# Kernel optimization log

Measured on AMD Instinct MI355X. Metric: run time of the kernel, lower is better.

## Reference

```python
import jax, jax.numpy as jnp
import numpy as np

N = 100000
E = 3200000
F_IN = 256
HID = 16
N_CLS = 32


def setup_inputs() -> dict:
    key = jax.random.key(0)
    ks = jax.random.split(key, 9)
    x = jax.random.normal(ks[0], (N, F_IN), dtype=jnp.float32)
    edge_index = jax.random.randint(ks[1], (2, E), 0, N, dtype=jnp.int32)
    def glorot(k, fan_in, fan_out):
        s = jnp.sqrt(6.0 / (fan_in + fan_out)).astype(jnp.float32)
        return jax.random.uniform(k, (fan_in, fan_out), jnp.float32, -s, s)
    return {
        "x": x,
        "edge_index": edge_index,
        "W1": glorot(ks[2], F_IN, HID), "b1": jnp.zeros((HID,), jnp.float32),
        "W2": glorot(ks[3], HID, HID), "b2": jnp.zeros((HID,), jnp.float32),
        "W3": glorot(ks[4], HID, N_CLS), "b3": jnp.zeros((N_CLS,), jnp.float32),
    }


def _gcn_conv(h, W, b, src, dst, deg_inv_sqrt):
    # h: [N, d_in] -> [N, d_out]. PyG GCNConv: linear, then D^-1/2 (A+I) D^-1/2 aggregation, then bias.
    h = h @ W                                        # [N, d_out]
    norm = deg_inv_sqrt[src] * deg_inv_sqrt[dst]     # [E]
    msg = h[src] * norm[:, None]                     # [E, d_out]
    agg = jax.ops.segment_sum(msg, dst, num_segments=N)
    # self-loop contribution: norm_ii = deg_inv_sqrt[i]^2
    agg = agg + (deg_inv_sqrt ** 2)[:, None] * h
    return agg + b


def reference(x, edge_index, W1, b1, W2, b2, W3, b3):
    src, dst = edge_index[0], edge_index[1]
    # degree with self-loops (edge weights = 1), computed on dst per PyG gcn_norm
    deg = jax.ops.segment_sum(jnp.ones((E,), jnp.float32), dst, num_segments=N) + 1.0
    deg_inv_sqrt = jax.lax.rsqrt(deg)
    h = jax.nn.elu(_gcn_conv(x, W1, b1, src, dst, deg_inv_sqrt))
    h = jax.nn.elu(_gcn_conv(h, W2, b2, src, dst, deg_inv_sqrt))
    h = jax.nn.elu(_gcn_conv(h, W3, b3, src, dst, deg_inv_sqrt))
    # dropout is identity in eval mode (training=False)
    return jax.nn.log_softmax(h, axis=1)
```

## Files before the change

kernel.cpp:

```cpp
#include <hip/hip_runtime.h>
#include <math.h>

static constexpr int N_NODES = 100000;
static constexpr int N_EDGES = 3200000;
static constexpr int F_INC   = 256;
static constexpr int HIDC    = 16;
static constexpr int NCLS    = 32;

static constexpr int BNODES  = 256;
static constexpr int NBKT    = (N_NODES + BNODES - 1) / BNODES;
static constexpr int CAP     = 9216;
static constexpr int CHUNK   = 4096;
static constexpr int NCHUNK  = (N_EDGES + CHUNK - 1) / CHUNK;
static constexpr int NTILES  = N_NODES / 16;
static constexpr int GLIN1   = (NTILES + 3) / 4;

typedef __attribute__((ext_vector_type(8))) short bf16x8;
typedef __attribute__((ext_vector_type(4))) float f32x4;

__device__ __forceinline__ unsigned pack_bf2(float a, float b) {
    unsigned ua = __float_as_uint(a);
    unsigned ub = __float_as_uint(b);
    ua = (ua + 0x7FFFu + ((ua >> 16) & 1u)) >> 16;
    ub = (ub + 0x7FFFu + ((ub >> 16) & 1u)) & 0xFFFF0000u;
    return ua | ub;
}
__device__ __forceinline__ float bflo(unsigned v) { return __uint_as_float(v << 16); }
__device__ __forceinline__ float bfhi(unsigned v) { return __uint_as_float(v & 0xFFFF0000u); }
__device__ __forceinline__ float elu1(float t) { return t > 0.f ? t : expm1f(t); }

__global__ void k_zero_cur(int* gcur) {
    int i = threadIdx.x;
    if (i < NBKT) gcur[i] = 0;
}

__global__ __launch_bounds__(256) void k_bucklin(const int* __restrict__ src,
                                                 const int* __restrict__ dst,
                                                 int* gcur, unsigned int* __restrict__ slab,
                                                 const float* __restrict__ x,
                                                 const float* __restrict__ W1,
                                                 unsigned* __restrict__ hb) {
    __shared__ int sm[8192];
    int tid = threadIdx.x;
    if (blockIdx.x < NCHUNK) {
        int* hist  = sm;
        int* sc    = sm + 512;
        int* place = sm + 1024;
        int* gbase = sm + 1536;
        unsigned* staging = (unsigned*)(sm + 2048);
        unsigned short* bid = (unsigned short*)(sm + 6144);
        int e0 = blockIdx.x * CHUNK;
        int n = min(CHUNK, N_EDGES - e0);
        hist[tid] = 0; hist[tid + 256] = 0;
        __syncthreads();
        unsigned pay[16];
        int bk[16];
        #pragma unroll
        for (int r = 0; r < 16; ++r) {
            int i = r * 256 + tid;
            bk[r] = -1;
            if (i < n) {
                int e = e0 + i;
                int s = src[e];
                int t = dst[e];
                int b = t >> 8;
                pay[r] = (unsigned)s | ((unsigned)(t & 255) << 24);
                bk[r] = b;
                atomicAdd(&hist[b], 1);
            }
        }
        __syncthreads();
        sc[tid] = hist[tid]; sc[tid + 256] = hist[tid + 256];
        __syncthreads();
        for (int off = 1; off < 512; off <<= 1) {
            int i0 = tid, i1 = tid + 256;
            int v0 = (i0 >= off) ? sc[i0 - off] : 0;
            int v1 = (i1 >= off) ? sc[i1 - off] : 0;
            __syncthreads();
            sc[i0] += v0; sc[i1] += v1;
            __syncthreads();
        }
        {
            int b0 = tid, b1 = tid + 256;
            int o0 = sc[b0] - hist[b0];
            int o1 = sc[b1] - hist[b1];
            place[b0] = o0; place[b1] = o1;
            sc[b0] = o0; sc[b1] = o1;
            if (b0 < NBKT && hist[b0]) gbase[b0] = atomicAdd(&gcur[b0], hist[b0]);
            if (b1 < NBKT && hist[b1]) gbase[b1] = atomicAdd(&gcur[b1], hist[b1]);
        }
        __syncthreads();
        #pragma unroll
        for (int r = 0; r < 16; ++r) {
            if (bk[r] >= 0) {
                int p = atomicAdd(&place[bk[r]], 1);
                staging[p] = pay[r];
                bid[p] = (unsigned short)bk[r];
            }
        }
        __syncthreads();
        for (int i = tid; i < n; i += 256) {
            int b = bid[i];
            int gp = gbase[b] + (i - sc[b]);
            if (gp < CAP) slab[(size_t)b * CAP + gp] = staging[i];
        }
    } else {
        float* dtile = (float*)sm;
        int lane = tid & 63;
        int w = tid >> 6;
        int tile = (blockIdx.x - NCHUNK) * 4 + w;
        if (tile >= NTILES) return;
        int g = lane >> 4;
        int r = lane & 15;
        union { uint4 u; bf16x8 v; } bfr[8];
        #pragma unroll
        for (int m = 0; m < 8; ++m) {
            unsigned uu[4];
            #pragma unroll
            for (int t = 0; t < 4; ++t) {
                int k0 = 32 * m + 8 * g + 2 * t;
                uu[t] = pack_bf2(W1[k0 * HIDC + r], W1[(k0 + 1) * HIDC + r]);
            }
            bfr[m].u = make_uint4(uu[0], uu[1], uu[2], uu[3]);
        }
        const float* xrow = x + (size_t)(tile * 16 + r) * F_INC;
        f32x4 acc = {0.f, 0.f, 0.f, 0.f};
        #pragma unroll
        for (int m = 0; m < 8; ++m) {
            int ks = 32 * m + 8 * g;
            float4 va = *(const float4*)(xrow + ks);
            float4 vb = *(const float4*)(xrow + ks + 4);
            union { uint4 u; bf16x8 v; } af;
            af.u = make_uint4(pack_bf2(va.x, va.y), pack_bf2(va.z, va.w),
                              pack_bf2(vb.x, vb.y), pack_bf2(vb.z, vb.w));
            acc = __builtin_amdgcn_mfma_f32_16x16x32_bf16(af.v, bfr[m].v, acc, 0, 0, 0);
        }
        float* dt = dtile + w * 288;
        #pragma unroll
        for (int t = 0; t < 4; ++t) dt[(4 * g + t) * 18 + r] = acc[t];
        __builtin_amdgcn_s_waitcnt(0);
        int q = lane & 7;
        #pragma unroll
        for (int h = 0; h < 2; ++h) {
            int rr = (lane >> 3) + 8 * h;
            int node = tile * 16 + rr;
            hb[(size_t)node * 8 + q] = pack_bf2(dt[rr * 18 + 2 * q], dt[rr * 18 + 2 * q + 1]);
        }
    }
}

__global__ __launch_bounds__(512) void k_csr(const int* __restrict__ gcur,
                                             unsigned int* __restrict__ slab,
                                             int* __restrict__ rowptr,
                                             int* __restrict__ cnt,
                                             float* __restrict__ dis) {
    __shared__ int hist[BNODES];
    __shared__ int lofs[BNODES];
    __shared__ int place[BNODES];
    __shared__ unsigned int reord[CAP];
    int tid = threadIdx.x, b = blockIdx.x;
    if (tid < BNODES) hist[tid] = 0;
    __syncthreads();
    int count = min(gcur[b], CAP);
    unsigned int* sl = slab + (size_t)b * CAP;
    for (int i = tid; i < count; i += 512) atomicAdd(&hist[sl[i] >> 24], 1);
    __syncthreads();
    if (tid < BNODES) lofs[tid] = hist[tid];
    __syncthreads();
    for (int off = 1; off < BNODES; off <<= 1) {
        int v = 0;
        if (tid < BNODES && tid >= off) v = lofs[tid - off];
        __syncthreads();
        if (tid < BNODES) lofs[tid] += v;
        __syncthreads();
    }
    if (tid < BNODES) {
        int ex = lofs[tid] - hist[tid];
        lofs[tid] = ex;
        place[tid] = ex;
        int node = b * BNODES + tid;
        if (node < N_NODES) {
            rowptr[node] = b * CAP + ex;
            cnt[node] = hist[tid];
            dis[node] = rsqrtf((float)hist[tid] + 1.0f);
        }
    }
    __syncthreads();
    for (int i = tid; i < count; i += 512) {
        unsigned int v = sl[i];
        int dl = v >> 24;
        int p = atomicAdd(&place[dl], 1);
        reord[p] = v & 0xFFFFFFu;
    }
    __syncthreads();
    for (int i = tid; i < count; i += 512) sl[i] = reord[i];
}

__device__ __forceinline__ void gather4(int base, int deg, int q,
                                        const unsigned* __restrict__ csr,
                                        const unsigned* __restrict__ hb,
                                        float& a0, float& a1, float& a2, float& a3) {
    int j = 0;
    for (; j + 3 < deg; j += 4) {
        int s0 = csr[base + j];
        int s1 = csr[base + j + 1];
        int s2 = csr[base + j + 2];
        int s3 = csr[base + j + 3];
        uint2 v0 = *(const uint2*)&hb[(size_t)s0 * 8 + 2 * q];
        uint2 v1 = *(const uint2*)&hb[(size_t)s1 * 8 + 2 * q];
        uint2 v2 = *(const uint2*)&hb[(size_t)s2 * 8 + 2 * q];
        uint2 v3 = *(const uint2*)&hb[(size_t)s3 * 8 + 2 * q];
        a0 += (bflo(v0.x) + bflo(v1.x)) + (bflo(v2.x) + bflo(v3.x));
        a1 += (bfhi(v0.x) + bfhi(v1.x)) + (bfhi(v2.x) + bfhi(v3.x));
        a2 += (bflo(v0.y) + bflo(v1.y)) + (bflo(v2.y) + bflo(v3.y));
        a3 += (bfhi(v0.y) + bfhi(v1.y)) + (bfhi(v2.y) + bfhi(v3.y));
    }
    for (; j < deg; ++j) {
        int s = csr[base + j];
        uint2 v = *(const uint2*)&hb[(size_t)s * 8 + 2 * q];
        a0 += bflo(v.x); a1 += bfhi(v.x); a2 += bflo(v.y); a3 += bfhi(v.y);
    }
}

__global__ __launch_bounds__(256) void k_gather_fl1(const int* __restrict__ rowptr,
                                                    const int* __restrict__ cnt,
                                                    const unsigned* __restrict__ csr,
                                                    const float* __restrict__ dis,
                                                    const unsigned* __restrict__ hb,
                                                    const float* __restrict__ b1,
                                                    const float* __restrict__ W2,
                                                    unsigned* __restrict__ hb_out) {
    __shared__ float W2s[HIDC * HIDC];
    __shared__ float b1s[HIDC];
    if (threadIdx.x < HIDC * HIDC) W2s[threadIdx.x] = W2[threadIdx.x];
    if (threadIdx.x < HIDC) b1s[threadIdx.x] = b1[threadIdx.x];
    __syncthreads();
    int idx = blockIdx.x * blockDim.x + threadIdx.x;
    int n = idx >> 2;
    if (n >= N_NODES) return;
    int q = idx & 3;
    int lane = threadIdx.x & 63;
    int base = rowptr[n];
    int deg = cnt[n];
    float dn = dis[n];
    uint2 sv = *(const uint2*)&hb[(size_t)n * 8 + 2 * q];
    float a0 = dn * bflo(sv.x), a1 = dn * bfhi(sv.x);
    float a2 = dn * bflo(sv.y), a3 = dn * bfhi(sv.y);
    int j = 0;
    for (; j + 3 < deg; j += 4) {
        int s0 = csr[base + j];
        int s1 = csr[base + j + 1];
        int s2 = csr[base + j + 2];
        int s3 = csr[base + j + 3];
        float d0 = dis[s0], d1 = dis[s1], d2 = dis[s2], d3 = dis[s3];
        uint2 v0 = *(const uint2*)&hb[(size_t)s0 * 8 + 2 * q];
        uint2 v1 = *(const uint2*)&hb[(size_t)s1 * 8 + 2 * q];
        uint2 v2 = *(const uint2*)&hb[(size_t)s2 * 8 + 2 * q];
        uint2 v3 = *(const uint2*)&hb[(size_t)s3 * 8 + 2 * q];
        a0 += d0 * bflo(v0.x) + d1 * bflo(v1.x) + d2 * bflo(v2.x) + d3 * bflo(v3.x);
        a1 += d0 * bfhi(v0.x) + d1 * bfhi(v1.x) + d2 * bfhi(v2.x) + d3 * bfhi(v3.x);
        a2 += d0 * bflo(v0.y) + d1 * bflo(v1.y) + d2 * bflo(v2.y) + d3 * bflo(v3.y);
        a3 += d0 * bfhi(v0.y) + d1 * bfhi(v1.y) + d2 * bfhi(v2.y) + d3 * bfhi(v3.y);
    }
    for (; j < deg; ++j) {
        int s = csr[base + j];
        float ds = dis[s];
        uint2 v = *(const uint2*)&hb[(size_t)s * 8 + 2 * q];
        a0 += ds * bflo(v.x); a1 += ds * bfhi(v.x);
        a2 += ds * bflo(v.y); a3 += ds * bfhi(v.y);
    }
    a0 = elu1(dn * a0 + b1s[4 * q + 0]);
    a1 = elu1(dn * a1 + b1s[4 * q + 1]);
    a2 = elu1(dn * a2 + b1s[4 * q + 2]);
    a3 = elu1(dn * a3 + b1s[4 * q + 3]);
    int gb = lane & 60;
    float h0 = 0.f, h1 = 0.f, h2 = 0.f, h3 = 0.f;
    #pragma unroll
    for (int kl = 0; kl < 4; ++kl) {
        float e0 = __shfl(a0, gb + kl, 64);
        float e1 = __shfl(a1, gb + kl, 64);
        float e2 = __shfl(a2, gb + kl, 64);
        float e3 = __shfl(a3, gb + kl, 64);
        const float* w0 = &W2s[(4 * kl) * HIDC + 4 * q];
        const float* w1 = &W2s[(4 * kl + 1) * HIDC + 4 * q];
        const float* w2 = &W2s[(4 * kl + 2) * HIDC + 4 * q];
        const float* w3 = &W2s[(4 * kl + 3) * HIDC + 4 * q];
        h0 += e0 * w0[0] + e1 * w1[0] + e2 * w2[0] + e3 * w3[0];
        h1 += e0 * w0[1] + e1 * w1[1] + e2 * w2[1] + e3 * w3[1];
        h2 += e0 * w0[2] + e1 * w1[2] + e2 * w2[2] + e3 * w3[2];
        h3 += e0 * w0[3] + e1 * w1[3] + e2 * w2[3] + e3 * w3[3];
    }
    *(uint2*)&hb_out[(size_t)n * 8 + 2 * q] =
        make_uint2(pack_bf2(dn * h0, dn * h1), pack_bf2(dn * h2, dn * h3));
}

__global__ __launch_bounds__(256) void k_gather_z(const int* __restrict__ rowptr,
                                                  const int* __restrict__ cnt,
                                                  const unsigned* __restrict__ csr,
                                                  const float* __restrict__ dis,
                                                  const unsigned* __restrict__ hb,
                                                  const float* __restrict__ bias,
                                                  unsigned* __restrict__ outp) {
    int idx = blockIdx.x * blockDim.x + threadIdx.x;
    int n = idx >> 2;
    if (n >= N_NODES) return;
    int q = idx & 3;
    uint2 sv = *(const uint2*)&hb[(size_t)n * 8 + 2 * q];
    float a0 = bflo(sv.x), a1 = bfhi(sv.x), a2 = bflo(sv.y), a3 = bfhi(sv.y);
    gather4(rowptr[n], cnt[n], q, csr, hb, a0, a1, a2, a3);
    float dn = dis[n];
    float z0 = elu1(a0 * dn + bias[4 * q + 0]);
    float z1 = elu1(a1 * dn + bias[4 * q + 1]);
    float z2 = elu1(a2 * dn + bias[4 * q + 2]);
    float z3 = elu1(a3 * dn + bias[4 * q + 3]);
    *(uint2*)&outp[(size_t)n * 8 + 2 * q] =
        make_uint2(pack_bf2(dn * z0, dn * z1), pack_bf2(dn * z2, dn * z3));
}

__global__ __launch_bounds__(256) void k_gather_fin(const int* __restrict__ rowptr,
                                                    const int* __restrict__ cnt,
                                                    const unsigned* __restrict__ csr,
                                                    const float* __restrict__ dis,
                                                    const unsigned* __restrict__ hb,
                                                    const float* __restrict__ W3,
                                                    const float* __restrict__ b3,
                                                    float* __restrict__ out) {
    __shared__ float W3s[HIDC * NCLS];
    __shared__ float b3s[NCLS];
    for (int i = threadIdx.x; i < HIDC * NCLS; i += 256) W3s[i] = W3[i];
    if (threadIdx.x < NCLS) b3s[threadIdx.x] = b3[threadIdx.x];
    __syncthreads();
    int idx = blockIdx.x * blockDim.x + threadIdx.x;
    int n = idx >> 2;
    if (n >= N_NODES) return;
    int q = idx & 3;
    int lane = threadIdx.x & 63;
    uint2 sv = *(const uint2*)&hb[(size_t)n * 8 + 2 * q];
    float a0 = bflo(sv.x), a1 = bfhi(sv.x), a2 = bflo(sv.y), a3 = bfhi(sv.y);
    gather4(rowptr[n], cnt[n], q, csr, hb, a0, a1, a2, a3);
    float dn = dis[n];
    a0 *= dn; a1 *= dn; a2 *= dn; a3 *= dn;
    int gb = lane & 60;
    int j0 = q * 8;
    float r[8];
    #pragma unroll
    for (int c = 0; c < 8; ++c) r[c] = b3s[j0 + c];
    #pragma unroll
    for (int kl = 0; kl < 4; ++kl) {
        float e0 = __shfl(a0, gb + kl, 64);
        float e1 = __shfl(a1, gb + kl, 64);
        float e2 = __shfl(a2, gb + kl, 64);
        float e3 = __shfl(a3, gb + kl, 64);
        const float* w0 = &W3s[(4 * kl) * NCLS + j0];
        const float* w1 = &W3s[(4 * kl + 1) * NCLS + j0];
        const float* w2 = &W3s[(4 * kl + 2) * NCLS + j0];
        const float* w3 = &W3s[(4 * kl + 3) * NCLS + j0];
        #pragma unroll
        for (int c = 0; c < 8; ++c)
            r[c] += e0 * w0[c] + e1 * w1[c] + e2 * w2[c] + e3 * w3[c];
    }
    float m = -1e30f;
    #pragma unroll
    for (int c = 0; c < 8; ++c) { r[c] = elu1(r[c]); m = fmaxf(m, r[c]); }
    m = fmaxf(m, __shfl_xor(m, 1, 64));
    m = fmaxf(m, __shfl_xor(m, 2, 64));
    float s = 0.f;
    #pragma unroll
    for (int c = 0; c < 8; ++c) s += expf(r[c] - m);
    s += __shfl_xor(s, 1, 64);
    s += __shfl_xor(s, 2, 64);
    float lse = logf(s) + m;
    float4* o = (float4*)(out + (size_t)n * NCLS + j0);
    o[0] = make_float4(r[0] - lse, r[1] - lse, r[2] - lse, r[3] - lse);
    o[1] = make_float4(r[4] - lse, r[5] - lse, r[6] - lse, r[7] - lse);
}

extern "C" void kernel_launch(void* const* d_in, const int* in_sizes, int n_in,
                              void* d_out, int out_size, void* d_ws, size_t ws_size,
                              hipStream_t stream) {
    const float* x  = (const float*)d_in[0];
    const int*   ei = (const int*)d_in[1];
    const float* W1 = (const float*)d_in[2];
    const float* b1 = (const float*)d_in[3];
    const float* W2 = (const float*)d_in[4];
    const float* b2 = (const float*)d_in[5];
    const float* W3 = (const float*)d_in[6];
    const float* b3 = (const float*)d_in[7];
    float* out = (float*)d_out;
    const int* src = ei;
    const int* dst = ei + N_EDGES;

    int* wi = (int*)d_ws;
    int*          gcur   = wi;
    unsigned int* slab   = (unsigned int*)(wi + 512);
    int*          rowptr = wi + 512 + NBKT * CAP;
    int*          cnt    = rowptr + 102400;
    float*        dis    = (float*)(cnt + 102400);
    unsigned*     Bh     = (unsigned*)(dis + 102400);
    unsigned*     Zb     = Bh + 819200;
    (void)ws_size; (void)n_in; (void)in_sizes; (void)out_size;

    const int GG4 = (int)(((long long)N_NODES * 4 + 255) / 256);

    k_zero_cur<<<1, 512, 0, stream>>>(gcur);
    k_bucklin<<<NCHUNK + GLIN1, 256, 0, stream>>>(src, dst, gcur, slab, x, W1, Bh);
    k_csr<<<NBKT, 512, 0, stream>>>(gcur, slab, rowptr, cnt, dis);

    k_gather_fl1<<<GG4, 256, 0, stream>>>(rowptr, cnt, slab, dis, Bh, b1, W2, Zb);
    k_gather_z<<<GG4, 256, 0, stream>>>(rowptr, cnt, slab, dis, Zb, b2, Bh);
    k_gather_fin<<<GG4, 256, 0, stream>>>(rowptr, cnt, slab, dis, Bh, W3, b3, out);
}
```

Before: 185.6 us.

## Split linear1 from bucketing and prescale features by source degree norm

Splits the fused bucket-and-linear kernel into separate bucketing and layer-1 linear kernels. The linear kernel now runs after the CSR build so it can multiply each node's projected features by dis[node] before storing them in bf16. That lets the first gather reuse the shared gather4 helper, which presumably drops the per-edge dis[src] lookup. The cost is one more kernel launch and losing the overlap of the GEMM with the edge bucketing.

```diff
diff --git a/kernel.cpp b/kernel.cpp
--- a/kernel.cpp
+++ b/kernel.cpp
@@ -34,118 +34,70 @@
     if (i < NBKT) gcur[i] = 0;
 }
 
-__global__ __launch_bounds__(256) void k_bucklin(const int* __restrict__ src,
-                                                 const int* __restrict__ dst,
-                                                 int* gcur, unsigned int* __restrict__ slab,
-                                                 const float* __restrict__ x,
-                                                 const float* __restrict__ W1,
-                                                 unsigned* __restrict__ hb) {
-    __shared__ int sm[8192];
+__global__ __launch_bounds__(256) void k_bucket(const int* __restrict__ src,
+                                                const int* __restrict__ dst,
+                                                int* gcur, unsigned int* __restrict__ slab) {
+    __shared__ int hist[512];
+    __shared__ int sc[512];
+    __shared__ int place[512];
+    __shared__ int gbase[512];
+    __shared__ unsigned int staging[CHUNK];
+    __shared__ unsigned short bid[CHUNK];
     int tid = threadIdx.x;
-    if (blockIdx.x < NCHUNK) {
-        int* hist  = sm;
-        int* sc    = sm + 512;
-        int* place = sm + 1024;
-        int* gbase = sm + 1536;
-        unsigned* staging = (unsigned*)(sm + 2048);
-        unsigned short* bid = (unsigned short*)(sm + 6144);
-        int e0 = blockIdx.x * CHUNK;
-        int n = min(CHUNK, N_EDGES - e0);
-        hist[tid] = 0; hist[tid + 256] = 0;
+    int e0 = blockIdx.x * CHUNK;
+    int n = min(CHUNK, N_EDGES - e0);
+    hist[tid] = 0; hist[tid + 256] = 0;
+    __syncthreads();
+    unsigned int pay[16];
+    int bk[16];
+    #pragma unroll
+    for (int r = 0; r < 16; ++r) {
+        int i = r * 256 + tid;
+        bk[r] = -1;
+        if (i < n) {
+            int e = e0 + i;
+            int s = src[e];
+            int t = dst[e];
+            int b = t >> 8;
+            pay[r] = (unsigned)s | ((unsigned)(t & 255) << 24);
+            bk[r] = b;
+            atomicAdd(&hist[b], 1);
+        }
+    }
+    __syncthreads();
+    sc[tid] = hist[tid]; sc[tid + 256] = hist[tid + 256];
+    __syncthreads();
+    for (int off = 1; off < 512; off <<= 1) {
+        int i0 = tid, i1 = tid + 256;
+        int v0 = (i0 >= off) ? sc[i0 - off] : 0;
+        int v1 = (i1 >= off) ? sc[i1 - off] : 0;
         __syncthreads();
-        unsigned pay[16];
-        int bk[16];
-        #pragma unroll
-        for (int r = 0; r < 16; ++r) {
-            int i = r * 256 + tid;
-            bk[r] = -1;
-            if (i < n) {
-                int e = e0 + i;
-                int s = src[e];
-                int t = dst[e];
-                int b = t >> 8;
-                pay[r] = (unsigned)s | ((unsigned)(t & 255) << 24);
-                bk[r] = b;
-                atomicAdd(&hist[b], 1);
-            }
+        sc[i0] += v0; sc[i1] += v1;
+        __syncthreads();
+    }
+    {
+        int b0 = tid, b1 = tid + 256;
+        int o0 = sc[b0] - hist[b0];
+        int o1 = sc[b1] - hist[b1];
+        place[b0] = o0; place[b1] = o1;
+        sc[b0] = o0; sc[b1] = o1;
+        if (b0 < NBKT && hist[b0]) gbase[b0] = atomicAdd(&gcur[b0], hist[b0]);
+        if (b1 < NBKT && hist[b1]) gbase[b1] = atomicAdd(&gcur[b1], hist[b1]);
+    }
+    __syncthreads();
+    #pragma unroll
+    for (int r = 0; r < 16; ++r) {
+        if (bk[r] >= 0) {
+            int p = atomicAdd(&place[bk[r]], 1);
+            staging[p] = pay[r];
+            bid[p] = (unsigned short)bk[r];
         }
-        __syncthreads();
-        sc[tid] = hist[tid]; sc[tid + 256] = hist[tid + 256];
-        __syncthreads();
-        for (int off = 1; off < 512; off <<= 1) {
-            int i0 = tid, i1 = tid + 256;
-            int v0 = (i0 >= off) ? sc[i0 - off] : 0;
-            int v1 = (i1 >= off) ? sc[i1 - off] : 0;
-            __syncthreads();
-            sc[i0] += v0; sc[i1] += v1;
-            __syncthreads();
-        }
-        {
-            int b0 = tid, b1 = tid + 256;
-            int o0 = sc[b0] - hist[b0];
-            int o1 = sc[b1] - hist[b1];
-            place[b0] = o0; place[b1] = o1;
-            sc[b0] = o0; sc[b1] = o1;
-            if (b0 < NBKT && hist[b0]) gbase[b0] = atomicAdd(&gcur[b0], hist[b0]);
-            if (b1 < NBKT && hist[b1]) gbase[b1] = atomicAdd(&gcur[b1], hist[b1]);
-        }
-        __syncthreads();
-        #pragma unroll
-        for (int r = 0; r < 16; ++r) {
-            if (bk[r] >= 0) {
-                int p = atomicAdd(&place[bk[r]], 1);
-                staging[p] = pay[r];
-                bid[p] = (unsigned short)bk[r];
-            }
-        }
-        __syncthreads();
-        for (int i = tid; i < n; i += 256) {
-            int b = bid[i];
-            int gp = gbase[b] + (i - sc[b]);
-            if (gp < CAP) slab[(size_t)b * CAP + gp] = staging[i];
-        }
-    } else {
-        float* dtile = (float*)sm;
-        int lane = tid & 63;
-        int w = tid >> 6;
-        int tile = (blockIdx.x - NCHUNK) * 4 + w;
-        if (tile >= NTILES) return;
-        int g = lane >> 4;
-        int r = lane & 15;
-        union { uint4 u; bf16x8 v; } bfr[8];
-        #pragma unroll
-        for (int m = 0; m < 8; ++m) {
-            unsigned uu[4];
-            #pragma unroll
-            for (int t = 0; t < 4; ++t) {
-                int k0 = 32 * m + 8 * g + 2 * t;
-                uu[t] = pack_bf2(W1[k0 * HIDC + r], W1[(k0 + 1) * HIDC + r]);
-            }
-            bfr[m].u = make_uint4(uu[0], uu[1], uu[2], uu[3]);
-        }
-        const float* xrow = x + (size_t)(tile * 16 + r) * F_INC;
-        f32x4 acc = {0.f, 0.f, 0.f, 0.f};
-        #pragma unroll
-        for (int m = 0; m < 8; ++m) {
-            int ks = 32 * m + 8 * g;
-            float4 va = *(const float4*)(xrow + ks);
-            float4 vb = *(const float4*)(xrow + ks + 4);
-            union { uint4 u; bf16x8 v; } af;
-            af.u = make_uint4(pack_bf2(va.x, va.y), pack_bf2(va.z, va.w),
-                              pack_bf2(vb.x, vb.y), pack_bf2(vb.z, vb.w));
-            acc = __builtin_amdgcn_mfma_f32_16x16x32_bf16(af.v, bfr[m].v, acc, 0, 0, 0);
-        }
-        float* dt = dtile + w * 288;
-        #pragma unroll
-        for (int t = 0; t < 4; ++t) dt[(4 * g + t) * 18 + r] = acc[t];
-        __builtin_amdgcn_s_waitcnt(0);
-        int q = lane & 7;
-        #pragma unroll
-        for (int h = 0; h < 2; ++h) {
-            int rr = (lane >> 3) + 8 * h;
-            int node = tile * 16 + rr;
-            hb[(size_t)node * 8 + q] = pack_bf2(dt[rr * 18 + 2 * q], dt[rr * 18 + 2 * q + 1]);
-        }
+    }
+    __syncthreads();
+    for (int i = tid; i < n; i += 256) {
+        int b = bid[i];
+        int gp = gbase[b] + (i - sc[b]);
+        if (gp < CAP) slab[(size_t)b * CAP + gp] = staging[i];
     }
 }
 
@@ -194,6 +146,55 @@
     }
     __syncthreads();
     for (int i = tid; i < count; i += 512) sl[i] = reord[i];
+}
+
+__global__ __launch_bounds__(256) void k_linear1(const float* __restrict__ x,
+                                                 const float* __restrict__ W1,
+                                                 const float* __restrict__ dis,
+                                                 unsigned* __restrict__ hb) {
+    __shared__ float dtile[4][16][18];
+    int tid = threadIdx.x;
+    int lane = tid & 63;
+    int w = tid >> 6;
+    int tile = blockIdx.x * 4 + w;
+    if (tile >= NTILES) return;
+    int g = lane >> 4;
+    int r = lane & 15;
+    union { uint4 u; bf16x8 v; } bfr[8];
+    #pragma unroll
+    for (int m = 0; m < 8; ++m) {
+        unsigned uu[4];
+        #pragma unroll
+        for (int t = 0; t < 4; ++t) {
+            int k0 = 32 * m + 8 * g + 2 * t;
+            uu[t] = pack_bf2(W1[k0 * HIDC + r], W1[(k0 + 1) * HIDC + r]);
+        }
+        bfr[m].u = make_uint4(uu[0], uu[1], uu[2], uu[3]);
+    }
+    const float* xrow = x + (size_t)(tile * 16 + r) * F_INC;
+    f32x4 acc = {0.f, 0.f, 0.f, 0.f};
+    #pragma unroll
+    for (int m = 0; m < 8; ++m) {
+        int ks = 32 * m + 8 * g;
+        float4 va = *(const float4*)(xrow + ks);
+        float4 vb = *(const float4*)(xrow + ks + 4);
+        union { uint4 u; bf16x8 v; } af;
+        af.u = make_uint4(pack_bf2(va.x, va.y), pack_bf2(va.z, va.w),
+                          pack_bf2(vb.x, vb.y), pack_bf2(vb.z, vb.w));
+        acc = __builtin_amdgcn_mfma_f32_16x16x32_bf16(af.v, bfr[m].v, acc, 0, 0, 0);
+    }
+    #pragma unroll
+    for (int t = 0; t < 4; ++t) dtile[w][4 * g + t][r] = acc[t];
+    __builtin_amdgcn_s_waitcnt(0);
+    int q = lane & 7;
+    #pragma unroll
+    for (int h = 0; h < 2; ++h) {
+        int rr = (lane >> 3) + 8 * h;
+        int node = tile * 16 + rr;
+        float dn = dis[node];
+        hb[(size_t)node * 8 + q] =
+            pack_bf2(dn * dtile[w][rr][2 * q], dn * dtile[w][rr][2 * q + 1]);
+    }
 }
 
 __device__ __forceinline__ void gather4(int base, int deg, int q,
@@ -240,39 +241,14 @@
     if (n >= N_NODES) return;
     int q = idx & 3;
     int lane = threadIdx.x & 63;
-    int base = rowptr[n];
-    int deg = cnt[n];
+    uint2 sv = *(const uint2*)&hb[(size_t)n * 8 + 2 * q];
+    float a0 = bflo(sv.x), a1 = bfhi(sv.x), a2 = bflo(sv.y), a3 = bfhi(sv.y);
+    gather4(rowptr[n], cnt[n], q, csr, hb, a0, a1, a2, a3);
     float dn = dis[n];
-    uint2 sv = *(const uint2*)&hb[(size_t)n * 8 + 2 * q];
-    float a0 = dn * bflo(sv.x), a1 = dn * bfhi(sv.x);
-    float a2 = dn * bflo(sv.y), a3 = dn * bfhi(sv.y);
-    int j = 0;
-    for (; j + 3 < deg; j += 4) {
-        int s0 = csr[base + j];
-        int s1 = csr[base + j + 1];
-        int s2 = csr[base + j + 2];
-        int s3 = csr[base + j + 3];
-        float d0 = dis[s0], d1 = dis[s1], d2 = dis[s2], d3 = dis[s3];
-        uint2 v0 = *(const uint2*)&hb[(size_t)s0 * 8 + 2 * q];
-        uint2 v1 = *(const uint2*)&hb[(size_t)s1 * 8 + 2 * q];
-        uint2 v2 = *(const uint2*)&hb[(size_t)s2 * 8 + 2 * q];
-        uint2 v3 = *(const uint2*)&hb[(size_t)s3 * 8 + 2 * q];
-        a0 += d0 * bflo(v0.x) + d1 * bflo(v1.x) + d2 * bflo(v2.x) + d3 * bflo(v3.x);
-        a1 += d0 * bfhi(v0.x) + d1 * bfhi(v1.x) + d2 * bfhi(v2.x) + d3 * bfhi(v3.x);
-        a2 += d0 * bflo(v0.y) + d1 * bflo(v1.y) + d2 * bflo(v2.y) + d3 * bflo(v3.y);
-        a3 += d0 * bfhi(v0.y) + d1 * bfhi(v1.y) + d2 * bfhi(v2.y) + d3 * bfhi(v3.y);
-    }
-    for (; j < deg; ++j) {
-        int s = csr[base + j];
-        float ds = dis[s];
-        uint2 v = *(const uint2*)&hb[(size_t)s * 8 + 2 * q];
-        a0 += ds * bflo(v.x); a1 += ds * bfhi(v.x);
-        a2 += ds * bflo(v.y); a3 += ds * bfhi(v.y);
-    }
-    a0 = elu1(dn * a0 + b1s[4 * q + 0]);
-    a1 = elu1(dn * a1 + b1s[4 * q + 1]);
-    a2 = elu1(dn * a2 + b1s[4 * q + 2]);
-    a3 = elu1(dn * a3 + b1s[4 * q + 3]);
+    a0 = elu1(a0 * dn + b1s[4 * q + 0]);
+    a1 = elu1(a1 * dn + b1s[4 * q + 1]);
+    a2 = elu1(a2 * dn + b1s[4 * q + 2]);
+    a3 = elu1(a3 * dn + b1s[4 * q + 3]);
     int gb = lane & 60;
     float h0 = 0.f, h1 = 0.f, h2 = 0.f, h3 = 0.f;
     #pragma unroll
@@ -403,9 +379,10 @@
     const int GG4 = (int)(((long long)N_NODES * 4 + 255) / 256);
 
     k_zero_cur<<<1, 512, 0, stream>>>(gcur);
-    k_bucklin<<<NCHUNK + GLIN1, 256, 0, stream>>>(src, dst, gcur, slab, x, W1, Bh);
+    k_bucket<<<NCHUNK, 256, 0, stream>>>(src, dst, gcur, slab);
     k_csr<<<NBKT, 512, 0, stream>>>(gcur, slab, rowptr, cnt, dis);
 
+    k_linear1<<<GLIN1, 256, 0, stream>>>(x, W1, dis, Bh);
     k_gather_fl1<<<GG4, 256, 0, stream>>>(rowptr, cnt, slab, dis, Bh, b1, W2, Zb);
     k_gather_z<<<GG4, 256, 0, stream>>>(rowptr, cnt, slab, dis, Zb, b2, Bh);
     k_gather_fin<<<GG4, 256, 0, stream>>>(rowptr, cnt, slab, dis, Bh, W3, b3, out);
```

Result: faster. 175.7 us (-5.3%).
